# Optimization experiments

Hardware: AMD Instinct MI355X
Metric: run time of the kernel (lower is better)

Reference implementation:

```python
import jax, jax.numpy as jnp
import numpy as np

N_STEPS = 2   # n_steps; n_head = 1 (module is only consistent for a single head)
NEG_SLOPE = 0.2


def setup_inputs() -> dict:
    key = jax.random.key(0)
    ks = jax.random.split(key, 6)
    B, C, N = 8, 2048, 2048  # N must equal input_dim (coefs*out broadcast requirement)
    s = 1.0 / np.sqrt(C).astype(np.float32)
    x = jax.random.normal(ks[0], (B, C, N), jnp.float32)
    Wa = jax.random.normal(ks[1], (C, C), jnp.float32) * s   # conv1x1, no bias
    Wb = jax.random.normal(ks[2], (C,), jnp.float32) * s     # conv1x1 -> 1 channel
    bb = jnp.zeros((1,), jnp.float32)
    Wc = jax.random.normal(ks[3], (C,), jnp.float32) * s
    bc = jnp.zeros((1,), jnp.float32)
    bias = jnp.zeros((C,), jnp.float32)                      # self.bias (zeros)
    return dict(x=x, Wa=Wa, Wb=Wb, bb=bb, Wc=Wc, bc=bc, bias=bias)


def _head_attention(out, Wa, Wb, bb, Wc, bc, bias):
    # dropout p=0.0 -> identity
    h = jnp.einsum('oc,bcn->bon', Wa, out)            # [B,C,N] conv1x1 projection
    t1 = jnp.einsum('c,bcn->bn', Wb, h) + bb          # [B,N]
    t2 = jnp.einsum('c,bcn->bn', Wc, h) + bc          # [B,N]
    z = t1[:, None, :] + t2[:, :, None]               # [B,N,N] additive outer-sum
    z = jnp.where(z >= 0, z, NEG_SLOPE * z)           # leaky_relu(0.2)
    # torch F.softmax with no dim on a 3D tensor uses legacy dim=0 (batch dim)
    coefs = jax.nn.softmax(z, axis=0)
    re = coefs * h + bias                             # bias broadcasts over last axis
    return re                                         # [B,N,N] (== [B,C,N] since N==C)


def reference(x, Wa, Wb, bb, Wc, bc, bias):
    out = x
    for _ in range(N_STEPS):
        # n_head == 1: stack of one head then mean is the head itself
        out = _head_attention(out, Wa, Wb, bb, Wc, bc, bias)
    return out
```

## Files before the change

kernel.cpp:

```cpp
#include <hip/hip_runtime.h>
#include <hip/hip_bf16.h>

typedef unsigned short ushort_t;
typedef __attribute__((ext_vector_type(8))) short bf16x8;
typedef __attribute__((ext_vector_type(4))) float f32x4;
typedef __attribute__((ext_vector_type(8))) unsigned short u16x8;
typedef __attribute__((ext_vector_type(4))) unsigned short u16x4;

#define NDIM 2048
#define BDIM 8

__device__ __forceinline__ float bf2f(unsigned short u) {
  union { unsigned int i; float f; } v; v.i = ((unsigned int)u) << 16; return v.f;
}
__device__ __forceinline__ unsigned short f2bf(float f) {
  union { float f; unsigned int i; } v; v.f = f;
  unsigned int x = v.i;
  x += 0x7fffu + ((x >> 16) & 1u);
  return (unsigned short)(x >> 16);
}

__device__ __forceinline__ void gload16(const void* g, void* l) {
  __builtin_amdgcn_global_load_lds(
      (const __attribute__((address_space(1))) void*)g,
      (__attribute__((address_space(3))) void*)l,
      16, 0, 0);
}

__global__ __launch_bounds__(256) void pack_a(const float* __restrict__ Wa,
                                              unsigned short* __restrict__ Apk) {
  const int sub = blockIdx.x * 4 + (threadIdx.x >> 6);
  const int l   = threadIdx.x & 63;
  const int mt  = sub >> 6, kt = sub & 63;
  const int fr  = l & 15, fs = l >> 4;
  const float* src = Wa + (size_t)(mt * 16 + fr) * NDIM + kt * 32 + fs * 8;
  f32x4 v0 = *(const f32x4*)&src[0];
  f32x4 v1 = *(const f32x4*)&src[4];
  u16x8 w;
  #pragma unroll
  for (int k = 0; k < 4; ++k) { w[k] = f2bf(v0[k]); w[4 + k] = f2bf(v1[k]); }
  *(u16x8*)&Apk[(size_t)sub * 512 + l * 8] = w;
}

__global__ __launch_bounds__(256) void transpose_convert(
    const float* __restrict__ x, unsigned short* __restrict__ dst,
    const float* __restrict__ wbe, const float* __restrict__ wce,
    float* __restrict__ t1, float* __restrict__ t2) {
  __shared__ float tile[64][65];
  const int b  = blockIdx.z;
  const int n0 = blockIdx.x * 64;
  const int c0 = blockIdx.y * 64;
  const int tr = threadIdx.x >> 4;
  const int tc = threadIdx.x & 15;
  const float* src = x + ((size_t)b * NDIM + c0) * NDIM + n0;
  #pragma unroll
  for (int p = 0; p < 4; ++p) {
    int r = p * 16 + tr;
    f32x4 v = *(const f32x4*)&src[(size_t)r * NDIM + tc * 4];
    #pragma unroll
    for (int k = 0; k < 4; ++k) tile[r][tc * 4 + k] = v[k];
  }
  __syncthreads();
  float w1[4], w2[4];
  #pragma unroll
  for (int k = 0; k < 4; ++k) {
    w1[k] = wbe[c0 + tc * 4 + k];
    w2[k] = wce[c0 + tc * 4 + k];
  }
  unsigned short* d = dst + ((size_t)b * NDIM + n0) * NDIM + c0;
  #pragma unroll
  for (int p = 0; p < 4; ++p) {
    int r = p * 16 + tr;
    u16x4 w;
    float a1 = 0.f, a2 = 0.f;
    #pragma unroll
    for (int k = 0; k < 4; ++k) {
      float v = tile[tc * 4 + k][r];
      w[k] = f2bf(v);
      a1 = fmaf(w1[k], v, a1);
      a2 = fmaf(w2[k], v, a2);
    }
    *(u16x4*)&d[(size_t)r * NDIM + tc * 4] = w;
    a1 += __shfl_xor(a1, 1); a1 += __shfl_xor(a1, 2);
    a1 += __shfl_xor(a1, 4); a1 += __shfl_xor(a1, 8);
    a2 += __shfl_xor(a2, 1); a2 += __shfl_xor(a2, 2);
    a2 += __shfl_xor(a2, 4); a2 += __shfl_xor(a2, 8);
    if (tc == 0) {
      atomicAdd(&t1[(size_t)b * NDIM + n0 + r], a1);
      atomicAdd(&t2[(size_t)b * NDIM + n0 + r], a2);
    }
  }
}

__global__ __launch_bounds__(256) void weff1(const float* __restrict__ Wa,
                                             const float* __restrict__ Wb,
                                             const float* __restrict__ Wc,
                                             float* __restrict__ part) {
  int c  = blockIdx.x * 256 + threadIdx.x;
  int o0 = blockIdx.y * 128;
  float ab = 0.f, ac = 0.f;
  for (int o = o0; o < o0 + 128; ++o) {
    float w = Wa[(size_t)o * NDIM + c];
    ab = fmaf(Wb[o], w, ab);
    ac = fmaf(Wc[o], w, ac);
  }
  part[(size_t)(blockIdx.y * 2 + 0) * NDIM + c] = ab;
  part[(size_t)(blockIdx.y * 2 + 1) * NDIM + c] = ac;
}
__global__ __launch_bounds__(256) void weff2(const float* __restrict__ part,
                                             float* __restrict__ wbe, float* __restrict__ wce) {
  int c = blockIdx.x * 256 + threadIdx.x;
  float ab = 0.f, ac = 0.f;
  #pragma unroll
  for (int i = 0; i < 16; ++i) {
    ab += part[(size_t)(i * 2 + 0) * NDIM + c];
    ac += part[(size_t)(i * 2 + 1) * NDIM + c];
  }
  wbe[c] = ab; wce[c] = ac;
}

__global__ __launch_bounds__(256) void s_kernel(const float* __restrict__ t1,
                                                const float* __restrict__ t2,
                                                const float* __restrict__ bb,
                                                const float* __restrict__ bc,
                                                float* __restrict__ S) {
  int n = blockIdx.x * 256 + threadIdx.x;
  int o = blockIdx.y;
  const float bias2 = bb[0] + bc[0];
  float acc = 0.f;
  #pragma unroll
  for (int b = 0; b < BDIM; ++b) {
    float z = t1[b * NDIM + n] + t2[b * NDIM + o] + bias2;
    z = z >= 0.f ? z : 0.2f * z;
    acc += __expf(z);
  }
  S[(size_t)o * NDIM + n] = __logf(acc);
}

__global__ __launch_bounds__(512, 2) void gemm_fused(
    const unsigned short* __restrict__ Apk,
    const unsigned short* __restrict__ Bt,
    const float* __restrict__ t1, const float* __restrict__ t2,
    const float* __restrict__ bb, const float* __restrict__ bc,
    const float* __restrict__ S,  const float* __restrict__ bias,
    const float* __restrict__ wbe, const float* __restrict__ wce,
    float* __restrict__ t1o, float* __restrict__ t2o,
    unsigned short* __restrict__ outT,
    float* __restrict__ outF,
    int write_f32) {
  __shared__ __align__(16) unsigned short sbuf[2][16384];

  const int tid  = threadIdx.x;
  const int lane = tid & 63;
  const int w    = tid >> 6;
  const int wr   = w >> 2;
  const int wc   = w & 3;
  const int bn0  = blockIdx.x * 256;
  const int bm0  = blockIdx.y * 256;
  const int bz   = blockIdx.z;
  const unsigned short* Bb = Bt + (size_t)bz * NDIM * NDIM;

  f32x4 acc[8][4];
  #pragma unroll
  for (int m = 0; m < 8; ++m)
    #pragma unroll
    for (int n = 0; n < 4; ++n) acc[m][n] = (f32x4){0.f, 0.f, 0.f, 0.f};

  const int sst   = (lane & 7) ^ (lane >> 3);
  const int srowl = lane >> 3;
  const unsigned short* bG = Bb + (size_t)(bn0 + w * 32 + srowl) * NDIM + sst * 8;
  auto stB = [&](int T, int p, int d) {
    gload16(bG + (size_t)p * 8 * NDIM + T * 64, &sbuf[d][(w * 32 + p * 8) * 64]);
  };

  const int fr  = lane & 15;
  const int fs  = lane >> 4;
  const int sl0 = ((fs) ^ (fr & 7)) * 8;
  const int sl1 = ((4 + fs) ^ (fr & 7)) * 8;
  const int bRow = (wc * 64 + fr) * 64;

  const unsigned int mtBase = (unsigned)((bm0 >> 4) + wr * 8);
  unsigned int aOff0[4], aOff1[4];
  #pragma unroll
  for (int m = 0; m < 4; ++m) {
    aOff0[m] = ((mtBase + m) * 64u) * 1024u + lane * 16u;
    aOff1[m] = ((mtBase + 4 + m) * 64u) * 1024u + lane * 16u;
  }

  bf16x8 Am0[4][2], Am1[4][2], bv[2][2];

  auto issueA = [&](bf16x8 (&dst)[4][2], const unsigned int (&off)[4]) {
    #pragma unroll
    for (int m = 0; m < 4; ++m) {
      asm volatile("global_load_dwordx4 %0, %1, %2"
                   : "=v"(dst[m][0]) : "v"(off[m]), "s"(Apk) : "memory");
      asm volatile("global_load_dwordx4 %0, %1, %2 offset:1024"
                   : "=v"(dst[m][1]) : "v"(off[m]), "s"(Apk) : "memory");
    }
  };
  auto rdB = [&](int nh, int d) {
    #pragma unroll
    for (int n = 0; n < 2; ++n) {
      const int base = d * 16384 + bRow + (nh * 2 + n) * 16 * 64;
      bv[n][0] = *(const bf16x8*)&sbuf[0][base + sl0];
      bv[n][1] = *(const bf16x8*)&sbuf[0][base + sl1];
    }
  };
  auto quad = [&](bf16x8 (&af)[4][2], int mo, int no) {
    __builtin_amdgcn_s_setprio(1);
    #pragma unroll
    for (int ks = 0; ks < 2; ++ks)
      #pragma unroll
      for (int m = 0; m < 4; ++m)
        #pragma unroll
        for (int n = 0; n < 2; ++n)
          acc[mo + m][no + n] = __builtin_amdgcn_mfma_f32_16x16x32_bf16(
              af[m][ks], bv[n][ks], acc[mo + m][no + n], 0, 0, 0);
    __builtin_amdgcn_s_setprio(0);
    __builtin_amdgcn_sched_barrier(0);
  };

  stB(0, 0, 0); stB(0, 1, 0); stB(0, 2, 0); stB(0, 3, 0);
  issueA(Am0, aOff0);
  asm volatile("s_waitcnt vmcnt(8)" ::: "memory");
  __builtin_amdgcn_s_barrier();

  #pragma clang loop unroll(disable)
  for (int tt = 0; tt < 16; ++tt) {
    const int Tn0 = 2 * tt + 1;
    const int Tn1 = (tt == 15) ? 31 : 2 * tt + 2;

    #pragma unroll
    for (int half = 0; half < 2; ++half) {
      const int cur = half, nxt = half ^ 1;
      const int Tn = half ? Tn1 : Tn0;

      issueA(Am1, aOff1);
      #pragma unroll
      for (int m = 0; m < 4; ++m) aOff1[m] += 2048u;
      rdB(0, cur);
      asm volatile("s_waitcnt vmcnt(8)" ::: "memory");
      __builtin_amdgcn_sched_barrier(0);
      quad(Am0, 0, 0);

      stB(Tn, 0, nxt); stB(Tn, 1, nxt);
      asm volatile("s_waitcnt vmcnt(2)" ::: "memory");
      __builtin_amdgcn_sched_barrier(0);
      quad(Am1, 4, 0);

      stB(Tn, 2, nxt); stB(Tn, 3, nxt);
      rdB(1, cur);
      #pragma unroll
      for (int m = 0; m < 4; ++m) aOff0[m] += 2048u;
      __builtin_amdgcn_sched_barrier(0);
      quad(Am0, 0, 2);

      issueA(Am0, aOff0);
      __builtin_amdgcn_sched_barrier(0);
      quad(Am1, 4, 2);

      asm volatile("s_waitcnt vmcnt(8)" ::: "memory");
      __builtin_amdgcn_s_barrier();
    }
  }

  asm volatile("s_waitcnt vmcnt(0)" ::: "memory");
  __syncthreads();

  float* sT1f = (float*)&sbuf[0][0];
  float* sT2f = sT1f + 256;
  if (tid < 256) sT1f[tid] = t1[bz * NDIM + bn0 + tid] + bb[0];
  else           sT2f[tid - 256] = t2[bz * NDIM + bm0 + (tid - 256)] + bc[0];
  __syncthreads();

  const int lr4 = fs * 4;
  if (write_f32) {
    #pragma unroll
    for (int m = 0; m < 8; ++m) {
      const int oo = wr * 128 + m * 16 + lr4;
      const int o  = bm0 + oo;
      #pragma unroll
      for (int n = 0; n < 4; ++n) {
        const int nn = wc * 64 + n * 16 + fr;
        const int ng = bn0 + nn;
        const float tz1  = sT1f[nn];
        const float bval = bias[ng];
        #pragma unroll
        for (int r = 0; r < 4; ++r) {
          float z = tz1 + sT2f[oo + r];
          z = z >= 0.f ? z : 0.2f * z;
          float coef = __expf(z - S[(size_t)(o + r) * NDIM + ng]);
          outF[(size_t)bz * NDIM * NDIM + (size_t)(o + r) * NDIM + ng] =
              fmaf(coef, acc[m][n][r], bval);
        }
      }
    }
  } else {
    float tp1[4] = {0.f, 0.f, 0.f, 0.f}, tp2[4] = {0.f, 0.f, 0.f, 0.f};
    #pragma unroll
    for (int m = 0; m < 8; ++m) {
      const int oo = wr * 128 + m * 16 + lr4;
      const int o  = bm0 + oo;
      float w1[4], w2[4];
      #pragma unroll
      for (int r = 0; r < 4; ++r) { w1[r] = wbe[o + r]; w2[r] = wce[o + r]; }
      #pragma unroll
      for (int n = 0; n < 4; ++n) {
        const int nn = wc * 64 + n * 16 + fr;
        const int ng = bn0 + nn;
        const float tz1  = sT1f[nn];
        const float bval = bias[ng];
        u16x4 wv;
        #pragma unroll
        for (int r = 0; r < 4; ++r) {
          float z = tz1 + sT2f[oo + r];
          z = z >= 0.f ? z : 0.2f * z;
          float coef = __expf(z - S[(size_t)(o + r) * NDIM + ng]);
          float val  = fmaf(coef, acc[m][n][r], bval);
          wv[r] = f2bf(val);
          tp1[n] = fmaf(w1[r], val, tp1[n]);
          tp2[n] = fmaf(w2[r], val, tp2[n]);
        }
        *(u16x4*)&outT[(size_t)bz * NDIM * NDIM + (size_t)ng * NDIM + o] = wv;
      }
    }
    #pragma unroll
    for (int n = 0; n < 4; ++n) {
      float a1 = tp1[n], a2 = tp2[n];
      a1 += __shfl_xor(a1, 16); a1 += __shfl_xor(a1, 32);
      a2 += __shfl_xor(a2, 16); a2 += __shfl_xor(a2, 32);
      if (fs == 0) {
        const int ng = bn0 + wc * 64 + n * 16 + fr;
        atomicAdd(&t1o[(size_t)bz * NDIM + ng], a1);
        atomicAdd(&t2o[(size_t)bz * NDIM + ng], a2);
      }
    }
  }
}

extern "C" void kernel_launch(void* const* d_in, const int* in_sizes, int n_in,
                              void* d_out, int out_size, void* d_ws, size_t ws_size,
                              hipStream_t stream) {
  const float* x    = (const float*)d_in[0];
  const float* Wa   = (const float*)d_in[1];
  const float* Wb   = (const float*)d_in[2];
  const float* bb   = (const float*)d_in[3];
  const float* Wc   = (const float*)d_in[4];
  const float* bc   = (const float*)d_in[5];
  const float* bias = (const float*)d_in[6];
  float* out = (float*)d_out;

  char* ws = (char*)d_ws;
  unsigned short* curA = (unsigned short*)ws; ws += (size_t)BDIM * NDIM * NDIM * 2;
  unsigned short* curB = (unsigned short*)ws; ws += (size_t)BDIM * NDIM * NDIM * 2;
  unsigned short* Apk  = (unsigned short*)ws; ws += (size_t)NDIM * NDIM * 2;
  float* t1a  = (float*)ws; ws += (size_t)BDIM * NDIM * 4;
  float* t2a  = (float*)ws; ws += (size_t)BDIM * NDIM * 4;
  float* t1b  = (float*)ws; ws += (size_t)BDIM * NDIM * 4;
  float* t2b  = (float*)ws; ws += (size_t)BDIM * NDIM * 4;
  float* wbe  = (float*)ws; ws += NDIM * 4;
  float* wce  = (float*)ws; ws += NDIM * 4;
  float* part = (float*)ws; ws += (size_t)32 * NDIM * 4;
  float* S    = (float*)ws; ws += (size_t)NDIM * NDIM * 4;

  hipMemsetAsync(t1a, 0, (size_t)4 * BDIM * NDIM * 4, stream);

  pack_a<<<2048, 256, 0, stream>>>(Wa, Apk);
  weff1<<<dim3(8, 16), 256, 0, stream>>>(Wa, Wb, Wc, part);
  weff2<<<8, 256, 0, stream>>>(part, wbe, wce);
  transpose_convert<<<dim3(32, 32, BDIM), 256, 0, stream>>>(x, curA, wbe, wce, t1a, t2a);

  s_kernel<<<dim3(NDIM / 256, NDIM), 256, 0, stream>>>(t1a, t2a, bb, bc, S);
  gemm_fused<<<dim3(8, 8, BDIM), 512, 0, stream>>>(
      Apk, curA, t1a, t2a, bb, bc, S, bias, wbe, wce, t1b, t2b, curB, out, 0);

  s_kernel<<<dim3(NDIM / 256, NDIM), 256, 0, stream>>>(t1b, t2b, bb, bc, S);
  gemm_fused<<<dim3(8, 8, BDIM), 512, 0, stream>>>(
      Apk, curB, t1b, t2b, bb, bc, S, bias, wbe, wce, t1a, t2a, curB, out, 1);
}
```

Before: 363.1 us.

## Fuse Wa packing with effective-weight reduction and hoist B stores in GEMM loop

Replaces the separate pack_a, weff1 and weff2 kernels with one prep kernel. It converts Wa to packed bf16 and, in the same pass, reduces Wb·Wa and Wc·Wa using wave shuffles and atomics into zeroed wbe/wce buffers, so Wa is read once instead of twice and two launches disappear. Inside the GEMM main loop, all four B-tile LDS stores are now issued up front and the vmcnt waits are relaxed, to overlap memory traffic with MFMA work. The atomics make the wbe/wce sums order-nondeterministic, and the prep grid launches only 128 blocks.

```diff
diff --git a/kernel.cpp b/kernel.cpp
--- a/kernel.cpp
+++ b/kernel.cpp
@@ -27,19 +27,56 @@
       16, 0, 0);
 }
 
-__global__ __launch_bounds__(256) void pack_a(const float* __restrict__ Wa,
-                                              unsigned short* __restrict__ Apk) {
-  const int sub = blockIdx.x * 4 + (threadIdx.x >> 6);
-  const int l   = threadIdx.x & 63;
-  const int mt  = sub >> 6, kt = sub & 63;
-  const int fr  = l & 15, fs = l >> 4;
-  const float* src = Wa + (size_t)(mt * 16 + fr) * NDIM + kt * 32 + fs * 8;
-  f32x4 v0 = *(const f32x4*)&src[0];
-  f32x4 v1 = *(const f32x4*)&src[4];
-  u16x8 w;
-  #pragma unroll
-  for (int k = 0; k < 4; ++k) { w[k] = f2bf(v0[k]); w[4 + k] = f2bf(v1[k]); }
-  *(u16x8*)&Apk[(size_t)sub * 512 + l * 8] = w;
+__global__ __launch_bounds__(256) void prep(const float* __restrict__ Wa,
+                                            const float* __restrict__ Wb,
+                                            const float* __restrict__ Wc,
+                                            unsigned short* __restrict__ Apk,
+                                            float* __restrict__ wbe,
+                                            float* __restrict__ wce) {
+  const int wv = threadIdx.x >> 6;
+  const int l  = threadIdx.x & 63;
+  const int fr = l & 15, fs = l >> 4;
+  const int mt0 = blockIdx.y * 8 + wv * 2;
+  const int o0  = mt0 * 16 + fr;
+  const int o1  = o0 + 16;
+  const float wb0 = Wb[o0], wb1 = Wb[o1];
+  const float wc0 = Wc[o0], wc1 = Wc[o1];
+  #pragma unroll
+  for (int kt = 0; kt < 8; ++kt) {
+    const int ktg = blockIdx.x * 8 + kt;
+    const float* s0 = Wa + (size_t)o0 * NDIM + ktg * 32 + fs * 8;
+    const float* s1 = Wa + (size_t)o1 * NDIM + ktg * 32 + fs * 8;
+    f32x4 a0 = *(const f32x4*)&s0[0], a1 = *(const f32x4*)&s0[4];
+    f32x4 b0 = *(const f32x4*)&s1[0], b1 = *(const f32x4*)&s1[4];
+    u16x8 w0, w1;
+    float p1[8], p2[8];
+    #pragma unroll
+    for (int j = 0; j < 4; ++j) {
+      w0[j] = f2bf(a0[j]); w0[4 + j] = f2bf(a1[j]);
+      w1[j] = f2bf(b0[j]); w1[4 + j] = f2bf(b1[j]);
+      p1[j]     = wb0 * a0[j] + wb1 * b0[j];
+      p1[4 + j] = wb0 * a1[j] + wb1 * b1[j];
+      p2[j]     = wc0 * a0[j] + wc1 * b0[j];
+      p2[4 + j] = wc0 * a1[j] + wc1 * b1[j];
+    }
+    *(u16x8*)&Apk[(size_t)(mt0 * 64 + ktg) * 512 + l * 8] = w0;
+    *(u16x8*)&Apk[(size_t)((mt0 + 1) * 64 + ktg) * 512 + l * 8] = w1;
+    #pragma unroll
+    for (int j = 0; j < 8; ++j) {
+      p1[j] += __shfl_xor(p1[j], 1); p1[j] += __shfl_xor(p1[j], 2);
+      p1[j] += __shfl_xor(p1[j], 4); p1[j] += __shfl_xor(p1[j], 8);
+      p2[j] += __shfl_xor(p2[j], 1); p2[j] += __shfl_xor(p2[j], 2);
+      p2[j] += __shfl_xor(p2[j], 4); p2[j] += __shfl_xor(p2[j], 8);
+    }
+    if (fr == 0) {
+      const int c = ktg * 32 + fs * 8;
+      #pragma unroll
+      for (int j = 0; j < 8; ++j) {
+        atomicAdd(&wbe[c + j], p1[j]);
+        atomicAdd(&wce[c + j], p2[j]);
+      }
+    }
+  }
 }
 
 __global__ __launch_bounds__(256) void transpose_convert(
@@ -90,33 +127,6 @@
       atomicAdd(&t2[(size_t)b * NDIM + n0 + r], a2);
     }
   }
-}
-
-__global__ __launch_bounds__(256) void weff1(const float* __restrict__ Wa,
-                                             const float* __restrict__ Wb,
-                                             const float* __restrict__ Wc,
-                                             float* __restrict__ part) {
-  int c  = blockIdx.x * 256 + threadIdx.x;
-  int o0 = blockIdx.y * 128;
-  float ab = 0.f, ac = 0.f;
-  for (int o = o0; o < o0 + 128; ++o) {
-    float w = Wa[(size_t)o * NDIM + c];
-    ab = fmaf(Wb[o], w, ab);
-    ac = fmaf(Wc[o], w, ac);
-  }
-  part[(size_t)(blockIdx.y * 2 + 0) * NDIM + c] = ab;
-  part[(size_t)(blockIdx.y * 2 + 1) * NDIM + c] = ac;
-}
-__global__ __launch_bounds__(256) void weff2(const float* __restrict__ part,
-                                             float* __restrict__ wbe, float* __restrict__ wce) {
-  int c = blockIdx.x * 256 + threadIdx.x;
-  float ab = 0.f, ac = 0.f;
-  #pragma unroll
-  for (int i = 0; i < 16; ++i) {
-    ab += part[(size_t)(i * 2 + 0) * NDIM + c];
-    ac += part[(size_t)(i * 2 + 1) * NDIM + c];
-  }
-  wbe[c] = ab; wce[c] = ac;
 }
 
 __global__ __launch_bounds__(256) void s_kernel(const float* __restrict__ t1,
@@ -238,17 +248,16 @@
       issueA(Am1, aOff1);
       #pragma unroll
       for (int m = 0; m < 4; ++m) aOff1[m] += 2048u;
+      stB(Tn, 0, nxt); stB(Tn, 1, nxt); stB(Tn, 2, nxt); stB(Tn, 3, nxt);
       rdB(0, cur);
-      asm volatile("s_waitcnt vmcnt(8)" ::: "memory");
+      asm volatile("s_waitcnt vmcnt(12)" ::: "memory");
       __builtin_amdgcn_sched_barrier(0);
       quad(Am0, 0, 0);
 
-      stB(Tn, 0, nxt); stB(Tn, 1, nxt);
-      asm volatile("s_waitcnt vmcnt(2)" ::: "memory");
+      asm volatile("s_waitcnt vmcnt(4)" ::: "memory");
       __builtin_amdgcn_sched_barrier(0);
       quad(Am1, 4, 0);
 
-      stB(Tn, 2, nxt); stB(Tn, 3, nxt);
       rdB(1, cur);
       #pragma unroll
       for (int m = 0; m < 4; ++m) aOff0[m] += 2048u;
@@ -360,14 +369,11 @@
   float* t2b  = (float*)ws; ws += (size_t)BDIM * NDIM * 4;
   float* wbe  = (float*)ws; ws += NDIM * 4;
   float* wce  = (float*)ws; ws += NDIM * 4;
-  float* part = (float*)ws; ws += (size_t)32 * NDIM * 4;
   float* S    = (float*)ws; ws += (size_t)NDIM * NDIM * 4;
 
-  hipMemsetAsync(t1a, 0, (size_t)4 * BDIM * NDIM * 4, stream);
-
-  pack_a<<<2048, 256, 0, stream>>>(Wa, Apk);
-  weff1<<<dim3(8, 16), 256, 0, stream>>>(Wa, Wb, Wc, part);
-  weff2<<<8, 256, 0, stream>>>(part, wbe, wce);
+  hipMemsetAsync(t1a, 0, ((size_t)4 * BDIM * NDIM + 2 * NDIM) * 4, stream);
+
+  prep<<<dim3(8, 16), 256, 0, stream>>>(Wa, Wb, Wc, Apk, wbe, wce);
   transpose_convert<<<dim3(32, 32, BDIM), 256, 0, stream>>>(x, curA, wbe, wce, t1a, t2a);
 
   s_kernel<<<dim3(NDIM / 256, NDIM), 256, 0, stream>>>(t1a, t2a, bb, bc, S);
```

Measured after the change: 384.5 us. 1.06x slower.
